# Optimization experiments

Measured on AMD Instinct MI355X. Metric: run time of the kernel, lower is better.

## Reference

```python
import jax, jax.numpy as jnp
import numpy as np

D = 1024
H = 16
HD = D // H


def setup_inputs() -> dict:
    key = jax.random.key(0)
    ks = jax.random.split(key, 12)
    s = 0.02
    return {
        "X": jax.random.normal(ks[0], (8, 1024, D), dtype=jnp.float32),
        "W_qkv": jax.random.normal(ks[1], (D, 3 * D), dtype=jnp.float32) * s,
        "b_qkv": jnp.zeros((3 * D,), dtype=jnp.float32),
        "W_out": jax.random.normal(ks[2], (D, D), dtype=jnp.float32) * s,
        "b_out": jnp.zeros((D,), dtype=jnp.float32),
        "ln1_g": jnp.ones((D,), dtype=jnp.float32),
        "ln1_b": jnp.zeros((D,), dtype=jnp.float32),
        "ln2_g": jnp.ones((D,), dtype=jnp.float32),
        "ln2_b": jnp.zeros((D,), dtype=jnp.float32),
        "W_ff1": jax.random.normal(ks[3], (D, 4 * D), dtype=jnp.float32) * s,
        "b_ff1": jnp.zeros((4 * D,), dtype=jnp.float32),
        "W_ff2": jax.random.normal(ks[4], (4 * D, D), dtype=jnp.float32) * s,
        "b_ff2": jnp.zeros((D,), dtype=jnp.float32),
    }


def _layer_norm(x, g, b, eps=1e-5):
    mu = jnp.mean(x, axis=-1, keepdims=True)
    var = jnp.var(x, axis=-1, keepdims=True)
    return (x - mu) * jax.lax.rsqrt(var + eps) * g + b


def reference(X, W_qkv, b_qkv, W_out, b_out, ln1_g, ln1_b, ln2_g, ln2_b,
              W_ff1, b_ff1, W_ff2, b_ff2):
    B, T, _ = X.shape
    qkv = X @ W_qkv + b_qkv                      # [B,T,3D]
    qkv = qkv.reshape(B, T, 3, H, HD).transpose(2, 0, 3, 1, 4)  # [3,B,H,T,hd]
    Q, K, V = qkv[0], qkv[1], qkv[2]
    scores = jnp.einsum("bhqd,bhkd->bhqk", Q, K) / np.sqrt(HD).astype(np.float32)
    attn = jax.nn.softmax(scores, axis=-1)
    ctx = jnp.einsum("bhqk,bhkd->bhqd", attn, V)  # [B,H,T,hd]
    ctx = ctx.transpose(0, 2, 1, 3).reshape(B, T, D)
    attn_out = ctx @ W_out + b_out
    X1 = _layer_norm(attn_out + X, ln1_g, ln1_b)
    ffn = jax.nn.gelu(X1 @ W_ff1 + b_ff1, approximate=False) @ W_ff2 + b_ff2
    return _layer_norm(ffn + X1, ln2_g, ln2_b)
```

## Files before the change

kernel.cpp:

```cpp
#include <hip/hip_runtime.h>
#include <hip/hip_bf16.h>
#include <cstdint>

typedef unsigned short u16;
typedef __bf16 bf16x8 __attribute__((ext_vector_type(8)));
typedef float f32x4 __attribute__((ext_vector_type(4)));

__device__ __forceinline__ u16 f2bf(float f) {
  unsigned int u = __float_as_uint(f);
  u += 0x7FFFu + ((u >> 16) & 1u);
  return (u16)(u >> 16);
}
__device__ __forceinline__ unsigned int pack2(float a, float b) {
  return (unsigned int)f2bf(a) | ((unsigned int)f2bf(b) << 16);
}

__global__ __launch_bounds__(256) void cast_bf16_k(const float* __restrict__ in,
                                                   u16* __restrict__ out) {
  const int i = (blockIdx.x * 256 + threadIdx.x) * 4;
  const float4 v = *(const float4*)(in + i);
  uint2 p;
  p.x = pack2(v.x, v.y);
  p.y = pack2(v.z, v.w);
  *(uint2*)(out + i) = p;
}

__global__ __launch_bounds__(256) void transpose_cast_k(const float* __restrict__ in,
                                                        u16* __restrict__ out,
                                                        int R, int C) {
  __shared__ float tile[32][33];
  const int bx = blockIdx.x * 32, by = blockIdx.y * 32;
  const int tx = threadIdx.x & 31, ty = threadIdx.x >> 5;
#pragma unroll
  for (int i = 0; i < 32; i += 8)
    tile[ty + i][tx] = in[(size_t)(by + ty + i) * C + (bx + tx)];
  __syncthreads();
#pragma unroll
  for (int i = 0; i < 32; i += 8)
    out[(size_t)(bx + ty + i) * R + (by + tx)] = f2bf(tile[tx][ty + i]);
}

#define BM 128
#define BN 128
#define BK 32

template <int EPI>
__global__ __launch_bounds__(256) void gemm_bt(
    const u16* __restrict__ A, const u16* __restrict__ Bt,
    const float* __restrict__ bias, const float* __restrict__ resid,
    float* __restrict__ out_f, u16* __restrict__ out_b,
    u16* __restrict__ q_out, u16* __restrict__ k_out, u16* __restrict__ vt_out,
    int M, int N, int K) {
  __shared__ u16 As[BM * BK];
  __shared__ u16 Bs[BN * BK];
  const int tid = threadIdx.x;
  const int wave = tid >> 6, lane = tid & 63;
  const int lhi = lane >> 4, llo = lane & 15;
  const int m0 = blockIdx.y * BM, n0 = blockIdx.x * BN;
  const int wr = (wave >> 1) * 64, wc = (wave & 1) * 64;

  f32x4 acc[4][4] = {};

  const int c0 = wave * 64 + lane;
  for (int k0 = 0; k0 < K; k0 += BK) {
    __syncthreads();
#pragma unroll
    for (int i = 0; i < 2; ++i) {
      const int c = c0 + i * 256;
      const int r = c >> 2, sub = c & 3;
      const u16* ga = A + (size_t)(m0 + r) * K + (k0 + sub * 8);
      const u16* gb = Bt + (size_t)(n0 + r) * K + (k0 + sub * 8);
      __builtin_amdgcn_global_load_lds(
          (const __attribute__((address_space(1))) unsigned int*)ga,
          (__attribute__((address_space(3))) unsigned int*)(As + (wave * 64 + i * 256) * 8),
          16, 0, 0);
      __builtin_amdgcn_global_load_lds(
          (const __attribute__((address_space(1))) unsigned int*)gb,
          (__attribute__((address_space(3))) unsigned int*)(Bs + (wave * 64 + i * 256) * 8),
          16, 0, 0);
    }
    __syncthreads();
    bf16x8 af[4], bfr[4];
#pragma unroll
    for (int mf = 0; mf < 4; ++mf)
      af[mf] = *(const bf16x8*)(As + (wr + mf * 16 + llo) * BK + lhi * 8);
#pragma unroll
    for (int nf = 0; nf < 4; ++nf)
      bfr[nf] = *(const bf16x8*)(Bs + (wc + nf * 16 + llo) * BK + lhi * 8);
#pragma unroll
    for (int mf = 0; mf < 4; ++mf)
#pragma unroll
      for (int nf = 0; nf < 4; ++nf)
        acc[mf][nf] =
            __builtin_amdgcn_mfma_f32_16x16x32_bf16(af[mf], bfr[nf], acc[mf][nf], 0, 0, 0);
  }

#pragma unroll
  for (int mf = 0; mf < 4; ++mf) {
#pragma unroll
    for (int nf = 0; nf < 4; ++nf) {
      const int col = n0 + wc + nf * 16 + llo;
      const int rowb = m0 + wr + mf * 16 + lhi * 4;
      const float bv = bias[col];
#pragma unroll
      for (int r = 0; r < 4; ++r) {
        const int row = rowb + r;
        const float v = acc[mf][nf][r] + bv;
        if (EPI == 0) {
          const int which = col >> 10, rem = col & 1023;
          const int h = rem >> 6, d = rem & 63;
          const int b = row >> 10, t = row & 1023;
          const size_t bh = (size_t)(b * 16 + h);
          const u16 u = f2bf(v);
          if (which == 0)
            q_out[(bh * 1024 + t) * 64 + d] = u;
          else if (which == 1)
            k_out[(bh * 1024 + t) * 64 + d] = u;
          else
            vt_out[(bh * 64 + d) * 1024 + t] = u;
        } else if (EPI == 1) {
          out_f[(size_t)row * N + col] = v + resid[(size_t)row * N + col];
        } else {
          const float gl = 0.5f * v * (1.0f + erff(v * 0.70710678118f));
          out_b[(size_t)row * N + col] = f2bf(gl);
        }
      }
    }
  }
}

__global__ __launch_bounds__(256) void attn_flash_k(const u16* __restrict__ Qb,
                                                    const u16* __restrict__ Kb,
                                                    const u16* __restrict__ Vt,
                                                    u16* __restrict__ ctx) {
  __shared__ char lds[8192 + 8192 + 4 * 2048];
  char* Ks = lds;
  char* Vs = lds + 8192;
  const int tid = threadIdx.x;
  const int wave = tid >> 6, lane = tid & 63;
  const int llo = lane & 15, lhi = lane >> 4;
  char* Ps = lds + 16384 + wave * 2048;
  const int bh = blockIdx.y;
  const int q0 = blockIdx.x * 64 + wave * 16;
  const size_t hq = (size_t)bh * 1024 * 64;
  const int swz = (llo & 7) << 4;

  const u16* qrow = Qb + hq + (size_t)(q0 + llo) * 64;
  const bf16x8 qf0 = *(const bf16x8*)(qrow + lhi * 8);
  const bf16x8 qf1 = *(const bf16x8*)(qrow + 32 + lhi * 8);

  f32x4 O[4] = {};
  float m = -3.0e38f, l = 0.f;
  const float C = 0.18033688011112042f;

  for (int t = 0; t < 16; ++t) {
    const int kv0 = t * 64;
    __syncthreads();
#pragma unroll
    for (int j = 0; j < 2; ++j) {
      const int p = (j * 256 + tid) * 16;
      const int r = p >> 7;
      const int c = (p & 127) ^ ((r & 7) << 4);
      const u16* gk = Kb + hq + (size_t)(kv0 + r) * 64 + (c >> 1);
      __builtin_amdgcn_global_load_lds(
          (const __attribute__((address_space(1))) unsigned int*)gk,
          (__attribute__((address_space(3))) unsigned int*)(Ks + (j * 256 + wave * 64) * 16),
          16, 0, 0);
      const u16* gv = Vt + (size_t)bh * 64 * 1024 + (size_t)r * 1024 + kv0 + (c >> 1);
      __builtin_amdgcn_global_load_lds(
          (const __attribute__((address_space(1))) unsigned int*)gv,
          (__attribute__((address_space(3))) unsigned int*)(Vs + (j * 256 + wave * 64) * 16),
          16, 0, 0);
    }
    __syncthreads();

    f32x4 s[4];
#pragma unroll
    for (int kt = 0; kt < 4; ++kt) {
      const int row = kt * 16 + llo;
      const bf16x8 k0 = *(const bf16x8*)(Ks + row * 128 + ((lhi * 16) ^ swz));
      const bf16x8 k1 = *(const bf16x8*)(Ks + row * 128 + ((64 + lhi * 16) ^ swz));
      f32x4 a = {};
      a = __builtin_amdgcn_mfma_f32_16x16x32_bf16(k0, qf0, a, 0, 0, 0);
      a = __builtin_amdgcn_mfma_f32_16x16x32_bf16(k1, qf1, a, 0, 0, 0);
      s[kt] = a;
    }

    float tmax = -3.0e38f;
#pragma unroll
    for (int kt = 0; kt < 4; ++kt)
#pragma unroll
      for (int r = 0; r < 4; ++r) tmax = fmaxf(tmax, s[kt][r]);
    tmax = fmaxf(tmax, __shfl_xor(tmax, 16));
    tmax = fmaxf(tmax, __shfl_xor(tmax, 32));
    const float mnew = fmaxf(m, tmax);
    const float sc = exp2f((m - mnew) * C);
    float tsum = 0.f;
#pragma unroll
    for (int kt = 0; kt < 4; ++kt)
#pragma unroll
      for (int r = 0; r < 4; ++r) {
        const float pv = exp2f((s[kt][r] - mnew) * C);
        s[kt][r] = pv;
        tsum += pv;
      }
    tsum += __shfl_xor(tsum, 16);
    tsum += __shfl_xor(tsum, 32);
    l = l * sc + tsum;
    m = mnew;
#pragma unroll
    for (int dt = 0; dt < 4; ++dt) O[dt] *= sc;

#pragma unroll
    for (int kt = 0; kt < 4; ++kt) {
      uint2 pk;
      pk.x = pack2(s[kt][0], s[kt][1]);
      pk.y = pack2(s[kt][2], s[kt][3]);
      *(uint2*)(Ps + llo * 128 + ((kt * 32 + lhi * 8) ^ swz)) = pk;
    }
    bf16x8 pb[2];
#pragma unroll
    for (int kc = 0; kc < 2; ++kc)
      pb[kc] = *(const bf16x8*)(Ps + llo * 128 + ((kc * 64 + lhi * 16) ^ swz));

#pragma unroll
    for (int dt = 0; dt < 4; ++dt) {
      const int vrow = dt * 16 + llo;
#pragma unroll
      for (int kc = 0; kc < 2; ++kc) {
        const bf16x8 vf = *(const bf16x8*)(Vs + vrow * 128 + ((kc * 64 + lhi * 16) ^ swz));
        O[dt] = __builtin_amdgcn_mfma_f32_16x16x32_bf16(vf, pb[kc], O[dt], 0, 0, 0);
      }
    }
  }

  const float inv = 1.0f / l;
  const int b = bh >> 4, h = bh & 15;
  u16* crow = ctx + ((size_t)(b * 1024 + q0 + llo)) * 1024 + h * 64;
#pragma unroll
  for (int dt = 0; dt < 4; ++dt) {
    uint2 pk;
    pk.x = pack2(O[dt][0] * inv, O[dt][1] * inv);
    pk.y = pack2(O[dt][2] * inv, O[dt][3] * inv);
    *(uint2*)(crow + dt * 16 + lhi * 4) = pk;
  }
}

__global__ __launch_bounds__(256) void layernorm_k(const float* __restrict__ y,
                                                   const float* __restrict__ g,
                                                   const float* __restrict__ be,
                                                   u16* __restrict__ out_b,
                                                   float* __restrict__ out_f) {
  const int row = blockIdx.x;
  const int t = threadIdx.x;
  const float* yr = y + (size_t)row * 1024;
  const float4 v = *(const float4*)(yr + t * 4);
  float s = v.x + v.y + v.z + v.w;
  float s2 = v.x * v.x + v.y * v.y + v.z * v.z + v.w * v.w;
#pragma unroll
  for (int m = 1; m < 64; m <<= 1) {
    s += __shfl_xor(s, m);
    s2 += __shfl_xor(s2, m);
  }
  __shared__ float red[8];
  const int wv = t >> 6, lane = t & 63;
  if (lane == 0) {
    red[wv * 2] = s;
    red[wv * 2 + 1] = s2;
  }
  __syncthreads();
  s = red[0] + red[2] + red[4] + red[6];
  s2 = red[1] + red[3] + red[5] + red[7];
  const float mu = s * (1.0f / 1024.0f);
  const float var = s2 * (1.0f / 1024.0f) - mu * mu;
  const float inv = rsqrtf(var + 1e-5f);
  const int c = t * 4;
  const float4 gg = *(const float4*)(g + c);
  const float4 bb = *(const float4*)(be + c);
  const float o0 = (v.x - mu) * inv * gg.x + bb.x;
  const float o1 = (v.y - mu) * inv * gg.y + bb.y;
  const float o2 = (v.z - mu) * inv * gg.z + bb.z;
  const float o3 = (v.w - mu) * inv * gg.w + bb.w;
  if (out_f) {
    float4 o = {o0, o1, o2, o3};
    *(float4*)(out_f + (size_t)row * 1024 + c) = o;
  }
  if (out_b) {
    uint2 p;
    p.x = pack2(o0, o1);
    p.y = pack2(o2, o3);
    *(uint2*)(out_b + (size_t)row * 1024 + c) = p;
  }
}

extern "C" void kernel_launch(void* const* d_in, const int* in_sizes, int n_in,
                              void* d_out, int out_size, void* d_ws, size_t ws_size,
                              hipStream_t stream) {
  const float* X = (const float*)d_in[0];
  const float* W_qkv = (const float*)d_in[1];
  const float* b_qkv = (const float*)d_in[2];
  const float* W_out = (const float*)d_in[3];
  const float* b_out = (const float*)d_in[4];
  const float* ln1_g = (const float*)d_in[5];
  const float* ln1_b = (const float*)d_in[6];
  const float* ln2_g = (const float*)d_in[7];
  const float* ln2_b = (const float*)d_in[8];
  const float* W_ff1 = (const float*)d_in[9];
  const float* b_ff1 = (const float*)d_in[10];
  const float* W_ff2 = (const float*)d_in[11];
  const float* b_ff2 = (const float*)d_in[12];

  char* ws = (char*)d_ws;
  size_t off = 0;
  auto alloc = [&](size_t bytes) {
    char* p = ws + off;
    off += (bytes + 255) & ~(size_t)255;
    return p;
  };
  u16* Xb = (u16*)alloc(8192ull * 1024 * 2);
  u16* Wqkvt = (u16*)alloc(3072ull * 1024 * 2);
  u16* Woutt = (u16*)alloc(1024ull * 1024 * 2);
  u16* Wff1t = (u16*)alloc(4096ull * 1024 * 2);
  u16* Wff2t = (u16*)alloc(1024ull * 4096 * 2);
  u16* Qb = (u16*)alloc(128ull * 1024 * 64 * 2);
  u16* Kb = (u16*)alloc(128ull * 1024 * 64 * 2);
  u16* Vtb = (u16*)alloc(128ull * 1024 * 64 * 2);
  u16* ctx = (u16*)alloc(8192ull * 1024 * 2);
  float* y1 = (float*)alloc(8192ull * 1024 * 4);
  u16* X1b = (u16*)alloc(8192ull * 1024 * 2);
  float* X1f = (float*)alloc(8192ull * 1024 * 4);
  u16* hbuf = Qb;

  cast_bf16_k<<<8192, 256, 0, stream>>>(X, Xb);
  transpose_cast_k<<<dim3(96, 32), 256, 0, stream>>>(W_qkv, Wqkvt, 1024, 3072);
  transpose_cast_k<<<dim3(32, 32), 256, 0, stream>>>(W_out, Woutt, 1024, 1024);
  transpose_cast_k<<<dim3(128, 32), 256, 0, stream>>>(W_ff1, Wff1t, 1024, 4096);
  transpose_cast_k<<<dim3(32, 128), 256, 0, stream>>>(W_ff2, Wff2t, 4096, 1024);

  gemm_bt<0><<<dim3(24, 64), 256, 0, stream>>>(Xb, Wqkvt, b_qkv, nullptr, nullptr, nullptr,
                                               Qb, Kb, Vtb, 8192, 3072, 1024);
  attn_flash_k<<<dim3(16, 128), 256, 0, stream>>>(Qb, Kb, Vtb, ctx);
  gemm_bt<1><<<dim3(8, 64), 256, 0, stream>>>(ctx, Woutt, b_out, X, y1, nullptr,
                                              nullptr, nullptr, nullptr, 8192, 1024, 1024);
  layernorm_k<<<8192, 256, 0, stream>>>(y1, ln1_g, ln1_b, X1b, X1f);
  gemm_bt<2><<<dim3(32, 64), 256, 0, stream>>>(X1b, Wff1t, b_ff1, nullptr, nullptr, hbuf,
                                               nullptr, nullptr, nullptr, 8192, 4096, 1024);
  gemm_bt<1><<<dim3(8, 64), 256, 0, stream>>>(hbuf, Wff2t, b_ff2, X1f, y1, nullptr,
                                              nullptr, nullptr, nullptr, 8192, 1024, 4096);
  layernorm_k<<<8192, 256, 0, stream>>>(y1, ln2_g, ln2_b, nullptr, (float*)d_out);
}
```

Measured before the change: 597.3 us.

## Replace GEMM with 256x256 double-buffered 8-wave pipelined kernel

Replaces the 128x128x32 single-buffered GEMM with a 256x256x64 tile kernel using 8 waves and double-buffered LDS. Global-to-LDS loads for upcoming k-tiles are interleaved with four MFMA phases, and the code uses an XOR-swizzled LDS layout, priority boosts around MFMA blocks and a block-index remap that spreads work across XCDs. The aim is to hide memory latency behind compute and cut LDS bank conflicts and synchronisation overhead. In exchange it uses 128KB of LDS per block and a large accumulator array, which limits occupancy, and the smaller grids (128 blocks for the N=1024 GEMMs) may underfill the GPU.

```diff
diff --git a/kernel.cpp b/kernel.cpp
--- a/kernel.cpp
+++ b/kernel.cpp
@@ -40,67 +40,116 @@
     out[(size_t)(bx + ty + i) * R + (by + tx)] = f2bf(tile[tx][ty + i]);
 }
 
-#define BM 128
-#define BN 128
-#define BK 32
-
 template <int EPI>
-__global__ __launch_bounds__(256) void gemm_bt(
+__global__ __launch_bounds__(512, 2) void gemm8(
     const u16* __restrict__ A, const u16* __restrict__ Bt,
     const float* __restrict__ bias, const float* __restrict__ resid,
     float* __restrict__ out_f, u16* __restrict__ out_b,
     u16* __restrict__ q_out, u16* __restrict__ k_out, u16* __restrict__ vt_out,
     int M, int N, int K) {
-  __shared__ u16 As[BM * BK];
-  __shared__ u16 Bs[BN * BK];
+  __shared__ char lds[131072];
   const int tid = threadIdx.x;
   const int wave = tid >> 6, lane = tid & 63;
-  const int lhi = lane >> 4, llo = lane & 15;
-  const int m0 = blockIdx.y * BM, n0 = blockIdx.x * BN;
-  const int wr = (wave >> 1) * 64, wc = (wave & 1) * 64;
-
-  f32x4 acc[4][4] = {};
-
-  const int c0 = wave * 64 + lane;
-  for (int k0 = 0; k0 < K; k0 += BK) {
-    __syncthreads();
-#pragma unroll
-    for (int i = 0; i < 2; ++i) {
-      const int c = c0 + i * 256;
-      const int r = c >> 2, sub = c & 3;
-      const u16* ga = A + (size_t)(m0 + r) * K + (k0 + sub * 8);
-      const u16* gb = Bt + (size_t)(n0 + r) * K + (k0 + sub * 8);
-      __builtin_amdgcn_global_load_lds(
-          (const __attribute__((address_space(1))) unsigned int*)ga,
-          (__attribute__((address_space(3))) unsigned int*)(As + (wave * 64 + i * 256) * 8),
-          16, 0, 0);
-      __builtin_amdgcn_global_load_lds(
-          (const __attribute__((address_space(1))) unsigned int*)gb,
-          (__attribute__((address_space(3))) unsigned int*)(Bs + (wave * 64 + i * 256) * 8),
-          16, 0, 0);
-    }
-    __syncthreads();
-    bf16x8 af[4], bfr[4];
-#pragma unroll
-    for (int mf = 0; mf < 4; ++mf)
-      af[mf] = *(const bf16x8*)(As + (wr + mf * 16 + llo) * BK + lhi * 8);
-#pragma unroll
-    for (int nf = 0; nf < 4; ++nf)
-      bfr[nf] = *(const bf16x8*)(Bs + (wc + nf * 16 + llo) * BK + lhi * 8);
-#pragma unroll
-    for (int mf = 0; mf < 4; ++mf)
-#pragma unroll
-      for (int nf = 0; nf < 4; ++nf)
-        acc[mf][nf] =
-            __builtin_amdgcn_mfma_f32_16x16x32_bf16(af[mf], bfr[nf], acc[mf][nf], 0, 0, 0);
-  }
-
-#pragma unroll
-  for (int mf = 0; mf < 4; ++mf) {
+  const int llo = lane & 15, lhi = lane >> 4;
+  const int wm = wave >> 2, wn = wave & 3;
+  const int NT = K >> 6;
+  const int nbx = N >> 8;
+  const int cpx = gridDim.x >> 3;
+  const int wg = (blockIdx.x & 7) * cpx + (blockIdx.x >> 3);
+  const int m0 = (wg / nbx) << 8, n0 = (wg % nbx) << 8;
+
+  const int rloc = tid >> 3;
+  const int scol = (((tid & 7) * 16) ^ ((rloc & 7) << 4)) >> 1;
+  const int swz = (llo & 7) << 4;
+
+  f32x4 acc[8][4] = {};
+  bf16x8 aF[2][4][2], bF[2][2][2];
+
+#define STAGE_A(tt, hi)                                                         \
+  if ((tt) < NT) {                                                              \
+    char* db_ = lds + (((tt) & 1) << 16);                                       \
+    _Pragma("unroll") for (int c_ = 0; c_ < 2; ++c_) {                          \
+      const u16* g_ =                                                           \
+          A + (size_t)(m0 + (hi) * 128 + c_ * 64 + rloc) * K + (tt) * 64 + scol;\
+      __builtin_amdgcn_global_load_lds(                                         \
+          (const __attribute__((address_space(1))) unsigned int*)g_,            \
+          (__attribute__((address_space(3))) unsigned int*)(db_ + (hi) * 16384 +\
+                                                           c_ * 8192 + wave * 1024), \
+          16, 0, 0);                                                            \
+    }                                                                           \
+  }
+
+#define STAGE_B(tt, hi)                                                         \
+  if ((tt) < NT) {                                                              \
+    char* db_ = lds + (((tt) & 1) << 16) + 32768;                               \
+    _Pragma("unroll") for (int c_ = 0; c_ < 2; ++c_) {                          \
+      const u16* g_ =                                                           \
+          Bt + (size_t)(n0 + (hi) * 128 + c_ * 64 + rloc) * K + (tt) * 64 + scol;\
+      __builtin_amdgcn_global_load_lds(                                         \
+          (const __attribute__((address_space(1))) unsigned int*)g_,            \
+          (__attribute__((address_space(3))) unsigned int*)(db_ + (hi) * 16384 +\
+                                                           c_ * 8192 + wave * 1024), \
+          16, 0, 0);                                                            \
+    }                                                                           \
+  }
+
+#define LOAD_A(mh)                                                              \
+  _Pragma("unroll") for (int mq_ = 0; mq_ < 4; ++mq_)                           \
+  _Pragma("unroll") for (int kk_ = 0; kk_ < 2; ++kk_)                           \
+    aF[mh][mq_][kk_] = *(const bf16x8*)(ldsA + (wm * 128 + (mh) * 64 + mq_ * 16 + llo) * 128 + \
+                                        ((kk_ * 64 + lhi * 16) ^ swz));
+
+#define LOAD_B(nh)                                                              \
+  _Pragma("unroll") for (int nf_ = 0; nf_ < 2; ++nf_)                           \
+  _Pragma("unroll") for (int kk_ = 0; kk_ < 2; ++kk_)                           \
+    bF[nh][nf_][kk_] = *(const bf16x8*)(ldsB + (wn * 64 + (nh) * 32 + nf_ * 16 + llo) * 128 + \
+                                        ((kk_ * 64 + lhi * 16) ^ swz));
+
+#define DO_MFMA(mh, nh)                                                         \
+  _Pragma("unroll") for (int mq_ = 0; mq_ < 4; ++mq_)                           \
+  _Pragma("unroll") for (int nf_ = 0; nf_ < 2; ++nf_)                           \
+  _Pragma("unroll") for (int kk_ = 0; kk_ < 2; ++kk_)                           \
+    acc[(mh) * 4 + mq_][(nh) * 2 + nf_] = __builtin_amdgcn_mfma_f32_16x16x32_bf16( \
+        aF[mh][mq_][kk_], bF[nh][nf_][kk_], acc[(mh) * 4 + mq_][(nh) * 2 + nf_], 0, 0, 0);
+
+#define SYNC_PRE                                      \
+  __builtin_amdgcn_s_barrier();                       \
+  asm volatile("s_waitcnt lgkmcnt(0)" ::: "memory");  \
+  __builtin_amdgcn_sched_barrier(0);                  \
+  __builtin_amdgcn_s_setprio(1);
+
+#define SYNC_POST                                     \
+  __builtin_amdgcn_s_setprio(0);                      \
+  __builtin_amdgcn_sched_barrier(0);                  \
+  __builtin_amdgcn_s_barrier();
+
+  STAGE_A(0, 0) STAGE_A(0, 1) STAGE_B(0, 0) STAGE_B(0, 1) STAGE_A(1, 0) STAGE_A(1, 1)
+  asm volatile("s_waitcnt vmcnt(4)" ::: "memory");
+  __builtin_amdgcn_s_barrier();
+
+  for (int t = 0; t < NT; ++t) {
+    const char* ldsA = lds + ((t & 1) << 16);
+    const char* ldsB = ldsA + 32768;
+    LOAD_A(0) LOAD_B(0)
+    STAGE_B(t + 1, 0)
+    SYNC_PRE DO_MFMA(0, 0) SYNC_POST
+    LOAD_A(1)
+    STAGE_B(t + 1, 1)
+    SYNC_PRE DO_MFMA(1, 0) SYNC_POST
+    LOAD_B(1)
+    STAGE_A(t + 2, 0)
+    SYNC_PRE DO_MFMA(0, 1) SYNC_POST
+    STAGE_A(t + 2, 1)
+    asm volatile("s_waitcnt vmcnt(4)" ::: "memory");
+    SYNC_PRE DO_MFMA(1, 1) SYNC_POST
+  }
+
+#pragma unroll
+  for (int mf = 0; mf < 8; ++mf) {
 #pragma unroll
     for (int nf = 0; nf < 4; ++nf) {
-      const int col = n0 + wc + nf * 16 + llo;
-      const int rowb = m0 + wr + mf * 16 + lhi * 4;
+      const int col = n0 + wn * 64 + nf * 16 + llo;
+      const int rowb = m0 + wm * 128 + mf * 16 + lhi * 4;
       const float bv = bias[col];
 #pragma unroll
       for (int r = 0; r < 4; ++r) {
@@ -109,15 +158,15 @@
         if (EPI == 0) {
           const int which = col >> 10, rem = col & 1023;
           const int h = rem >> 6, d = rem & 63;
-          const int b = row >> 10, t = row & 1023;
+          const int b = row >> 10, tq = row & 1023;
           const size_t bh = (size_t)(b * 16 + h);
           const u16 u = f2bf(v);
           if (which == 0)
-            q_out[(bh * 1024 + t) * 64 + d] = u;
+            q_out[(bh * 1024 + tq) * 64 + d] = u;
           else if (which == 1)
-            k_out[(bh * 1024 + t) * 64 + d] = u;
+            k_out[(bh * 1024 + tq) * 64 + d] = u;
           else
-            vt_out[(bh * 64 + d) * 1024 + t] = u;
+            vt_out[(bh * 64 + d) * 1024 + tq] = u;
         } else if (EPI == 1) {
           out_f[(size_t)row * N + col] = v + resid[(size_t)row * N + col];
         } else {
@@ -127,6 +176,13 @@
       }
     }
   }
+#undef STAGE_A
+#undef STAGE_B
+#undef LOAD_A
+#undef LOAD_B
+#undef DO_MFMA
+#undef SYNC_PRE
+#undef SYNC_POST
 }
 
 __global__ __launch_bounds__(256) void attn_flash_k(const u16* __restrict__ Qb,
@@ -337,15 +393,15 @@
   transpose_cast_k<<<dim3(128, 32), 256, 0, stream>>>(W_ff1, Wff1t, 1024, 4096);
   transpose_cast_k<<<dim3(32, 128), 256, 0, stream>>>(W_ff2, Wff2t, 4096, 1024);
 
-  gemm_bt<0><<<dim3(24, 64), 256, 0, stream>>>(Xb, Wqkvt, b_qkv, nullptr, nullptr, nullptr,
-                                               Qb, Kb, Vtb, 8192, 3072, 1024);
+  gemm8<0><<<384, 512, 0, stream>>>(Xb, Wqkvt, b_qkv, nullptr, nullptr, nullptr,
+                                    Qb, Kb, Vtb, 8192, 3072, 1024);
   attn_flash_k<<<dim3(16, 128), 256, 0, stream>>>(Qb, Kb, Vtb, ctx);
-  gemm_bt<1><<<dim3(8, 64), 256, 0, stream>>>(ctx, Woutt, b_out, X, y1, nullptr,
-                                              nullptr, nullptr, nullptr, 8192, 1024, 1024);
+  gemm8<1><<<128, 512, 0, stream>>>(ctx, Woutt, b_out, X, y1, nullptr,
+                                    nullptr, nullptr, nullptr, 8192, 1024, 1024);
   layernorm_k<<<8192, 256, 0, stream>>>(y1, ln1_g, ln1_b, X1b, X1f);
-  gemm_bt<2><<<dim3(32, 64), 256, 0, stream>>>(X1b, Wff1t, b_ff1, nullptr, nullptr, hbuf,
-                                               nullptr, nullptr, nullptr, 8192, 4096, 1024);
-  gemm_bt<1><<<dim3(8, 64), 256, 0, stream>>>(hbuf, Wff2t, b_ff2, X1f, y1, nullptr,
-                                              nullptr, nullptr, nullptr, 8192, 1024, 4096);
+  gemm8<2><<<512, 512, 0, stream>>>(X1b, Wff1t, b_ff1, nullptr, nullptr, hbuf,
+                                    nullptr, nullptr, nullptr, 8192, 4096, 1024);
+  gemm8<1><<<128, 512, 0, stream>>>(hbuf, Wff2t, b_ff2, X1f, y1, nullptr,
+                                    nullptr, nullptr, nullptr, 8192, 1024, 4096);
   layernorm_k<<<8192, 256, 0, stream>>>(y1, ln2_g, ln2_b, nullptr, (float*)d_out);
 }
```

New measurement: 613.0 us. 1.03x slower.
